# Performance work log

Hardware: AMD Instinct MI355X
Metric: run time of the kernel (lower is better)

Reference implementation:

```python
import jax, jax.numpy as jnp
from jax import lax
import numpy as np

B, T, D_IN, H, OUT = 64, 512, 512, 1024, 128


def setup_inputs() -> dict:
    key = jax.random.key(0)
    ks = jax.random.split(key, 12)
    s = 0.02
    return {
        "x": jax.random.normal(ks[0], (B, T, D_IN), dtype=jnp.float32),
        "W_ih0": jax.random.normal(ks[1], (H, D_IN), dtype=jnp.float32) * s,
        "W_hh0": jax.random.normal(ks[2], (H, H), dtype=jnp.float32) * s,
        "b_ih0": jax.random.normal(ks[3], (H,), dtype=jnp.float32) * s,
        "b_hh0": jax.random.normal(ks[4], (H,), dtype=jnp.float32) * s,
        "W_ih1": jax.random.normal(ks[5], (H, H), dtype=jnp.float32) * s,
        "W_hh1": jax.random.normal(ks[6], (H, H), dtype=jnp.float32) * s,
        "b_ih1": jax.random.normal(ks[7], (H,), dtype=jnp.float32) * s,
        "b_hh1": jax.random.normal(ks[8], (H,), dtype=jnp.float32) * s,
        "W_fc": jax.random.normal(ks[9], (OUT, H), dtype=jnp.float32) * s,
        "b_fc": jax.random.normal(ks[10], (OUT,), dtype=jnp.float32) * s,
    }


def _rnn_layer(seq, W_ih, W_hh, b_ih, b_hh):
    # seq: [B, T, D] -> outputs [B, T, H]; h_t = tanh(x_t W_ih^T + b_ih + h_{t-1} W_hh^T + b_hh)
    pre = jnp.einsum("btd,hd->bth", seq, W_ih) + b_ih + b_hh  # one big input GEMM
    h0 = jnp.zeros((seq.shape[0], W_hh.shape[0]), dtype=seq.dtype)

    def step(h, p_t):
        h_new = jnp.tanh(p_t + h @ W_hh.T)
        return h_new, h_new

    _, hs = lax.scan(step, h0, jnp.swapaxes(pre, 0, 1))  # [T, B, H]
    return jnp.swapaxes(hs, 0, 1)  # [B, T, H]


def reference(x, W_ih0, W_hh0, b_ih0, b_hh0, W_ih1, W_hh1, b_ih1, b_hh1, W_fc, b_fc):
    h1 = _rnn_layer(x, W_ih0, W_hh0, b_ih0, b_hh0)
    h2 = _rnn_layer(h1, W_ih1, W_hh1, b_ih1, b_hh1)
    last = h2[:, -1, :]  # [B, H]
    return last @ W_fc.T + b_fc  # [B, OUT]
```

## Files before the change

### kernel.cpp

```cpp
#include <hip/hip_runtime.h>
#include <stdint.h>
#include <stddef.h>

#define Bn   64
#define Tn   512
#define DINn 512
#define Hn   1024
#define OUTn 128

typedef __attribute__((ext_vector_type(4))) float f32x4;
typedef __attribute__((ext_vector_type(8))) short short8;
typedef __attribute__((ext_vector_type(4))) unsigned int u32x4;

__device__ __forceinline__ unsigned short f2bf(float f){
  unsigned int x = __builtin_bit_cast(unsigned int, f);
  x += 0x7fffu + ((x >> 16) & 1u);
  return (unsigned short)(x >> 16);
}
__device__ __forceinline__ float bf2f(unsigned short u){
  return __builtin_bit_cast(float, (unsigned int)u << 16);
}
__device__ __forceinline__ float tanh_fast(float v){
  float e = __expf(2.0f * v);
  return 1.0f - 2.0f / (e + 1.0f);
}

#define LGKM_BAR() asm volatile("s_waitcnt lgkmcnt(0)\ns_barrier" ::: "memory")

template<bool FAST>
__device__ __forceinline__ void st16(unsigned short* p, u32x4 v){
  if constexpr (FAST)
    asm volatile("global_store_dwordx4 %0, %1, off sc0" :: "v"(p), "v"(v) : "memory");
  else
    asm volatile("global_store_dwordx4 %0, %1, off sc0 sc1" :: "v"(p), "v"(v) : "memory");
}
__device__ __forceinline__ unsigned atom_poll(unsigned int* p){
  unsigned old, zero = 0;
  asm volatile("global_atomic_add %0, %1, %2, off sc0\n\t"
               "s_waitcnt vmcnt(0)"
               : "=&v"(old) : "v"(p), "v"(zero) : "memory");
  return old;
}
__device__ __forceinline__ void atom_poll2(unsigned int* p1, unsigned int* p2,
                                           unsigned &v1, unsigned &v2){
  unsigned zero = 0;
  asm volatile("global_atomic_add %0, %2, %4, off sc0\n\t"
               "global_atomic_add %1, %3, %4, off sc0\n\t"
               "s_waitcnt vmcnt(0)"
               : "=&v"(v1), "=&v"(v2)
               : "v"(p1), "v"(p2), "v"(zero) : "memory");
}
__device__ __forceinline__ void atom_inc(unsigned int* p){
  unsigned one = 1;
  asm volatile("global_atomic_add %0, %1, off" :: "v"(p), "v"(one) : "memory");
}
__device__ __forceinline__ unsigned ld1_sc0(const unsigned int* p){
  unsigned v;
  asm volatile("global_load_dword %0, %1, off sc0\n\t"
               "s_waitcnt vmcnt(0)" : "=&v"(v) : "v"(p) : "memory");
  return v;
}
__device__ __forceinline__ unsigned ld1_nt(const unsigned int* p){
  unsigned v;
  asm volatile("global_load_dword %0, %1, off nt\n\t"
               "s_waitcnt vmcnt(0)" : "=&v"(v) : "v"(p) : "memory");
  return v;
}
__device__ __forceinline__ void ld2_nt(const unsigned int* p1, const unsigned int* p2,
                                       unsigned &v1, unsigned &v2){
  asm volatile("global_load_dword %0, %2, off nt\n\t"
               "global_load_dword %1, %3, off nt\n\t"
               "s_waitcnt vmcnt(0)"
               : "=&v"(v1), "=&v"(v2) : "v"(p1), "v"(p2) : "memory");
}
__device__ __forceinline__ unsigned umin4(u32x4 a){
  unsigned m0 = a[0] < a[1] ? a[0] : a[1];
  unsigned m1 = a[2] < a[3] ? a[2] : a[3];
  return m0 < m1 ? m0 : m1;
}
__device__ __forceinline__ unsigned ld_line8_slow(const unsigned int* p){
  u32x4 a, b;
  asm volatile("global_load_dwordx4 %0, %2, off sc0 sc1\n\t"
               "global_load_dwordx4 %1, %3, off sc0 sc1\n\t"
               "s_waitcnt vmcnt(0)"
               : "=&v"(a), "=&v"(b) : "v"(p), "v"(p + 4) : "memory");
  unsigned ma = umin4(a), mb = umin4(b);
  return ma < mb ? ma : mb;
}
__device__ __forceinline__ void waitw_nt(const unsigned int* p, unsigned want){
  if (!want) return;
  for (int i = 0; i < (1 << 16); ++i){
    if (ld1_nt(p) >= want) return;
    if (i > 16) __builtin_amdgcn_s_sleep(1);
  }
}
__device__ __forceinline__ void waitw_nt2(const unsigned int* p1, unsigned w1,
                                          const unsigned int* p2, unsigned w2){
  if (!w1){ waitw_nt(p2, w2); return; }
  for (int i = 0; i < (1 << 16); ++i){
    unsigned v1, v2;
    ld2_nt(p1, p2, v1, v2);
    if (v1 >= w1 && v2 >= w2) return;
    if (i > 16) __builtin_amdgcn_s_sleep(1);
  }
}
template<bool FAST>
__device__ __forceinline__ void wait_one(unsigned int* fc, unsigned int* fl, unsigned wfast, unsigned wslow){
  if constexpr (FAST){
    if (!wfast) return;
    for (int i = 0; i < (1 << 16); ++i){
      if (atom_poll(fc) >= wfast) return;
      if (i > 8) __builtin_amdgcn_s_sleep(1);
    }
  } else {
    if (!wslow) return;
    for (int i = 0; i < (1 << 16); ++i){
      if (ld_line8_slow(fl) >= wslow) return;
      if (i > 16) __builtin_amdgcn_s_sleep(1);
    }
  }
}
template<bool FAST>
__device__ __forceinline__ void wait_dual(unsigned int* fc1, unsigned int* fl1, unsigned wf1, unsigned ws1,
                                          unsigned int* fc2, unsigned int* fl2, unsigned wf2, unsigned ws2){
  if constexpr (FAST){
    if (!wf2){ wait_one<true>(fc1, fl1, wf1, ws1); return; }
    for (int i = 0; i < (1 << 16); ++i){
      unsigned v1, v2;
      atom_poll2(fc1, fc2, v1, v2);
      if (v1 >= wf1 && v2 >= wf2) return;
      if (i > 8) __builtin_amdgcn_s_sleep(1);
    }
  } else {
    if (!ws2){ wait_one<false>(fc1, fl1, wf1, ws1); return; }
    for (int i = 0; i < (1 << 16); ++i){
      if (ld_line8_slow(fl1) >= ws1 && ld_line8_slow(fl2) >= ws2) return;
      if (i > 16) __builtin_amdgcn_s_sleep(1);
    }
  }
}

__device__ __forceinline__ bool chk8(u32x4 v){
  bool ok = true;
#pragma unroll
  for (int d = 0; d < 4; ++d){
    ok = ok && ((v[d] & 0xFFFFu) != 0xFFFFu) && ((v[d] >> 16) != 0xFFFFu);
  }
  return ok;
}
__device__ __forceinline__ void poison_stage(const unsigned short* src, unsigned short* dst, int lane){
  const unsigned short* p0 = src + lane*8;
  const unsigned short* p1 = p0 + 512;
  u32x4 v0, v1;
  bool ok = false;
  for (int i = 0; i < (1 << 16) && !ok; ++i){
    asm volatile("global_load_dwordx4 %0, %2, off nt\n\t"
                 "global_load_dwordx4 %1, %3, off nt\n\t"
                 "s_waitcnt vmcnt(0)"
                 : "=&v"(v0), "=&v"(v1) : "v"(p0), "v"(p1) : "memory");
    ok = chk8(v0) && chk8(v1);
    if (!ok && i > 4) __builtin_amdgcn_s_sleep(1);
  }
  *(u32x4*)(dst + lane*8) = v0;
  *(u32x4*)(dst + lane*8 + 512) = v1;
}
__device__ __forceinline__ void poison_pv(const unsigned short* p, float* pv, bool active){
  unsigned u0 = 0, u1 = 0, u2 = 0, u3 = 0;
  bool ok = !active;
  for (int i = 0; i < (1 << 16) && !ok; ++i){
    asm volatile("global_load_ushort %0, %4, off nt\n\t"
                 "global_load_ushort %1, %5, off nt\n\t"
                 "global_load_ushort %2, %6, off nt\n\t"
                 "global_load_ushort %3, %7, off nt\n\t"
                 "s_waitcnt vmcnt(0)"
                 : "=&v"(u0), "=&v"(u1), "=&v"(u2), "=&v"(u3)
                 : "v"(p), "v"(p + 8), "v"(p + 16), "v"(p + 24) : "memory");
    ok = (u0 != 0xFFFFu) && (u1 != 0xFFFFu) && (u2 != 0xFFFFu) && (u3 != 0xFFFFu);
    if (!ok && i > 4) __builtin_amdgcn_s_sleep(1);
  }
  pv[0] = bf2f((unsigned short)u0); pv[1] = bf2f((unsigned short)u1);
  pv[2] = bf2f((unsigned short)u2); pv[3] = bf2f((unsigned short)u3);
}

__device__ __forceinline__ void stage_pw(const unsigned short* src, unsigned short* dst, int lane){
  const unsigned short* p0 = src + lane*8;
  const unsigned short* p1 = p0 + 512;
  u32x4 v0, v1;
  asm volatile("global_load_dwordx4 %0, %2, off sc0\n\t"
               "global_load_dwordx4 %1, %3, off sc0\n\t"
               "s_waitcnt vmcnt(0)"
               : "=&v"(v0), "=&v"(v1) : "v"(p0), "v"(p1) : "memory");
  *(u32x4*)(dst + lane*8) = v0;
  *(u32x4*)(dst + lane*8 + 512) = v1;
}
__device__ __forceinline__ void stage_pw_pv(const unsigned short* src, unsigned short* dst, int lane,
                                            const unsigned short* p4, float* pv){
  const unsigned short* p0 = src + lane*8;
  const unsigned short* p1 = p0 + 512;
  u32x4 v0, v1; unsigned u0,u1,u2,u3;
  asm volatile(
    "global_load_dwordx4 %0, %6, off sc0\n\t"
    "global_load_dwordx4 %1, %7, off sc0\n\t"
    "global_load_ushort %2, %8, off sc0\n\t"
    "global_load_ushort %3, %9, off sc0\n\t"
    "global_load_ushort %4, %10, off sc0\n\t"
    "global_load_ushort %5, %11, off sc0\n\t"
    "s_waitcnt vmcnt(0)"
    : "=&v"(v0),"=&v"(v1),"=&v"(u0),"=&v"(u1),"=&v"(u2),"=&v"(u3)
    : "v"(p0),"v"(p1),"v"(p4),"v"(p4+8),"v"(p4+16),"v"(p4+24) : "memory");
  *(u32x4*)(dst + lane*8) = v0;
  *(u32x4*)(dst + lane*8 + 512) = v1;
  pv[0]=bf2f((unsigned short)u0); pv[1]=bf2f((unsigned short)u1);
  pv[2]=bf2f((unsigned short)u2); pv[3]=bf2f((unsigned short)u3);
}

template<bool FAST>
__device__ __forceinline__ void stage_lin(const unsigned short* base, unsigned short* hl, int tid){
  const unsigned short* p0 = base + (size_t)tid * 8;
  const unsigned short* p1 = p0 + 4096;
  u32x4 v0, v1;
  if constexpr (FAST)
    asm volatile("global_load_dwordx4 %0, %2, off sc0\n\t"
                 "global_load_dwordx4 %1, %3, off sc0\n\t"
                 "s_waitcnt vmcnt(0)"
                 : "=&v"(v0), "=&v"(v1) : "v"(p0), "v"(p1) : "memory");
  else
    asm volatile("global_load_dwordx4 %0, %2, off sc0 sc1\n\t"
                 "global_load_dwordx4 %1, %3, off sc0 sc1\n\t"
                 "s_waitcnt vmcnt(0)"
                 : "=&v"(v0), "=&v"(v1) : "v"(p0), "v"(p1) : "memory");
  *(u32x4*)((char*)hl + tid * 16) = v0;
  *(u32x4*)((char*)hl + tid * 16 + 8192) = v1;
}
template<bool FAST>
__device__ __forceinline__ void ld4_chunk(const unsigned short* p, float* pv){
  unsigned u0,u1,u2,u3;
  if constexpr (FAST)
    asm volatile("global_load_ushort %0, %4, off sc0\n\t"
                 "global_load_ushort %1, %5, off sc0\n\t"
                 "global_load_ushort %2, %6, off sc0\n\t"
                 "global_load_ushort %3, %7, off sc0\n\t"
                 "s_waitcnt vmcnt(0)"
                 : "=&v"(u0), "=&v"(u1), "=&v"(u2), "=&v"(u3)
                 : "v"(p), "v"(p + 8), "v"(p + 16), "v"(p + 24) : "memory");
  else
    asm volatile("global_load_ushort %0, %4, off sc0 sc1\n\t"
                 "global_load_ushort %1, %5, off sc0 sc1\n\t"
                 "global_load_ushort %2, %6, off sc0 sc1\n\t"
                 "global_load_ushort %3, %7, off sc0 sc1\n\t"
                 "s_waitcnt vmcnt(0)"
                 : "=&v"(u0), "=&v"(u1), "=&v"(u2), "=&v"(u3)
                 : "v"(p), "v"(p + 8), "v"(p + 16), "v"(p + 24) : "memory");
  pv[0] = bf2f((unsigned short)u0); pv[1] = bf2f((unsigned short)u1);
  pv[2] = bf2f((unsigned short)u2); pv[3] = bf2f((unsigned short)u3);
}

__device__ __forceinline__ f32x4 mfma_tile(const char* lbase, const short8* wf, int lrow, int kh){
  f32x4 a0 = {0.f,0.f,0.f,0.f}, a1 = a0, a2 = a0, a3 = a0;
  int rb = kh * 128 + lrow * 16;
#pragma unroll
  for (int kk = 0; kk < 8; ++kk)
    a0 = __builtin_amdgcn_mfma_f32_16x16x32_bf16(*(const short8*)(lbase + kk*512 + rb), wf[kk], a0, 0,0,0);
#pragma unroll
  for (int kk = 8; kk < 16; ++kk)
    a1 = __builtin_amdgcn_mfma_f32_16x16x32_bf16(*(const short8*)(lbase + kk*512 + rb), wf[kk], a1, 0,0,0);
#pragma unroll
  for (int kk = 16; kk < 24; ++kk)
    a2 = __builtin_amdgcn_mfma_f32_16x16x32_bf16(*(const short8*)(lbase + kk*512 + rb), wf[kk], a2, 0,0,0);
#pragma unroll
  for (int kk = 24; kk < 32; ++kk)
    a3 = __builtin_amdgcn_mfma_f32_16x16x32_bf16(*(const short8*)(lbase + kk*512 + rb), wf[kk], a3, 0,0,0);
  return (a0 + a1) + (a2 + a3);
}

__global__ void cvt_bf16x8(const float* __restrict__ in, unsigned short* __restrict__ out,
                           long long n8){
  long long i = (long long)blockIdx.x * blockDim.x + threadIdx.x;
  long long stride = (long long)gridDim.x * blockDim.x;
  for (; i < n8; i += stride){
    const float* p = in + i*8;
    float4 a = *(const float4*)p;
    float4 b = *(const float4*)(p+4);
    short8 v;
    v[0]=(short)f2bf(a.x); v[1]=(short)f2bf(a.y); v[2]=(short)f2bf(a.z); v[3]=(short)f2bf(a.w);
    v[4]=(short)f2bf(b.x); v[5]=(short)f2bf(b.y); v[6]=(short)f2bf(b.z); v[7]=(short)f2bf(b.w);
    *(short8*)(out + i*8) = v;
  }
}

__global__ void bias_combine(const float* __restrict__ a, const float* __restrict__ b, float* __restrict__ o,
                             const float* __restrict__ c, const float* __restrict__ d, float* __restrict__ p){
  int i = blockIdx.x * blockDim.x + threadIdx.x;
  if (i < Hn){ o[i] = a[i] + b[i]; p[i] = c[i] + d[i]; }
}

__launch_bounds__(256, 2)
__global__ void gemm_pre0(const float* __restrict__ Av, const unsigned short* __restrict__ Bm,
                          const float* __restrict__ bias, unsigned short* __restrict__ C,
                          int N, int K)
{
  __shared__ unsigned short lA[128*64];
  __shared__ unsigned short lB[128*64];
  int bn = blockIdx.x, bm = blockIdx.y;
  int m0 = bm*128, n0 = bn*128;
  int tid = threadIdx.x, lane = tid & 63, w = tid >> 6;
  int wm = (w >> 1)*64, wn = (w & 1)*64;
  int cl = lane & 15, kh = lane >> 4;

  f32x4 acc[4][4];
  f32x4 z = {0.f,0.f,0.f,0.f};
#pragma unroll
  for (int i=0;i<4;i++)
#pragma unroll
    for (int j=0;j<4;j++) acc[i][j]=z;

  for (int k0 = 0; k0 < K; k0 += 64){
    __syncthreads();
#pragma unroll
    for (int r = 0; r < 4; ++r){
      int c = r*256 + tid;
      int row = c >> 3, cof = (c & 7)*8;
      const float* ap = Av + (size_t)(m0+row)*K + k0 + cof;
      float4 a = *(const float4*)ap;
      float4 b = *(const float4*)(ap+4);
      short8 v;
      v[0]=(short)f2bf(a.x); v[1]=(short)f2bf(a.y); v[2]=(short)f2bf(a.z); v[3]=(short)f2bf(a.w);
      v[4]=(short)f2bf(b.x); v[5]=(short)f2bf(b.y); v[6]=(short)f2bf(b.z); v[7]=(short)f2bf(b.w);
      *(short8*)&lA[row*64 + cof] = v;
      const unsigned short* bp = Bm + (size_t)(n0+row)*K + k0 + cof;
      *(short8*)&lB[row*64 + cof] = *(const short8*)bp;
    }
    __syncthreads();
#pragma unroll
    for (int kk = 0; kk < 2; ++kk){
      int kb = kk*32 + kh*8;
      short8 af[4], bfr[4];
#pragma unroll
      for (int i=0;i<4;i++) af[i]  = *(const short8*)&lA[(wm + i*16 + cl)*64 + kb];
#pragma unroll
      for (int j=0;j<4;j++) bfr[j] = *(const short8*)&lB[(wn + j*16 + cl)*64 + kb];
#pragma unroll
      for (int i=0;i<4;i++)
#pragma unroll
        for (int j=0;j<4;j++)
          acc[i][j] = __builtin_amdgcn_mfma_f32_16x16x32_bf16(af[i], bfr[j], acc[i][j], 0,0,0);
    }
  }
#pragma unroll
  for (int j=0;j<4;j++){
    int n = n0 + wn + j*16 + cl;
    float bs = bias[n];
#pragma unroll
    for (int i=0;i<4;i++){
      int mr = m0 + wm + i*16 + kh*4;
#pragma unroll
      for (int e=0;e<4;e++){
        int m = mr + e;
        int b = m >> 9, t = m & (Tn-1);
        C[((size_t)t*Bn + b)*N + n] = f2bf(acc[i][j][e] + bs);
      }
    }
  }
}

template<int MODE, bool POISON>
__device__ __forceinline__ void rnn_body(
    int role, int g, int slot, int tid, int w, int lane, int cl, int kh, int lrow,
    const unsigned short* pre0, unsigned short* h1base, unsigned short* pre1base,
    unsigned short* h2base, const float* bias1,
    unsigned int* FCA0, unsigned int* FCA1, unsigned int* FCB, unsigned int* FCC,
    unsigned int* FLA, unsigned int* FLB, unsigned int* FLC,
    unsigned int* FNA, unsigned int* FNB, unsigned int* FNC,
    const short8* wf, unsigned short* hl, unsigned short* outl)
{
  constexpr bool FAST = (MODE < 2);
  const char* lbase = (const char*)hl;
  int n0 = slot*128 + w*16;
  int olocal = w*128 + ((cl>>3)*8 + kh*4)*8 + (cl&7);
  int khc = kh & 1;
  unsigned int* myFL = ((role == 0) ? FLA : (role == 1) ? FLB : FLC) + slot;
  unsigned int* myFN = ((role == 0) ? FNA : (role == 1) ? FNB : FNC) + slot;

  for (int t = 0; t < Tn; ++t){
    float pv[4] = {0.f,0.f,0.f,0.f};
    if (role == 0 && kh < 2){
      const unsigned short* pp = pre0 + ((size_t)t*Bn + g*8 + kh*4)*Hn + n0 + cl;
#pragma unroll
      for (int j=0;j<4;j++) pv[j] = bf2f(pp[(size_t)j*Hn]);
    }
    bool staged = true;
    if constexpr (MODE == 0 && POISON){
      if (role == 0){
        if (t > 0) poison_stage(h1base + ((size_t)(t+1)*8 + g)*8192 + w*1024, hl + w*1024, lane);
        else staged = false;
      } else if (role == 1){
        poison_stage(h1base + ((size_t)(t+2)*8 + g)*8192 + w*1024, hl + w*1024, lane);
      } else {
        const unsigned short* pA = pre1base + ((size_t)t*8 + g)*8192 + slot*1024
                                   + ((w*16+cl)>>3)*64 + khc*32 + (cl&7);
        if (t > 0) poison_stage(h2base + ((size_t)(t-1)*8 + g)*8192 + w*1024, hl + w*1024, lane);
        else staged = false;
        poison_pv(pA, pv, kh < 2);
      }
    } else if constexpr (MODE == 0){
      if (role == 0){
        if (t > 0){
          waitw_nt(FNA + w, (unsigned)t);
          stage_pw(h1base + ((size_t)(t+1)*8 + g)*8192 + w*1024, hl + w*1024, lane);
        } else staged = false;
      } else if (role == 1){
        waitw_nt(FNA + w, (unsigned)(t+1));
        stage_pw(h1base + ((size_t)(t+2)*8 + g)*8192 + w*1024, hl + w*1024, lane);
      } else {
        const unsigned short* pA = pre1base + ((size_t)t*8 + g)*8192 + slot*1024
                                   + ((w*16+cl)>>3)*64 + khc*32 + (cl&7);
        if (t > 0){
          waitw_nt2(FNC + w, (unsigned)t, FNB + slot, (unsigned)(t+1));
          stage_pw_pv(h2base + ((size_t)(t-1)*8 + g)*8192 + w*1024, hl + w*1024, lane, pA, pv);
        } else {
          staged = false;
          waitw_nt(FNB + slot, 1u);
          ld4_chunk<true>(pA, pv);
        }
      }
    } else {
      if (tid == 0){
        if (role == 0)      wait_one <FAST>(FCA0, FLA, 8u*(unsigned)t, (unsigned)t);
        else if (role == 1) wait_one <FAST>(FCA1, FLA, 8u*(unsigned)(t+1), (unsigned)(t+1));
        else                wait_dual<FAST>(FCB, FLB, 8u*(unsigned)(t+1), (unsigned)(t+1),
                                            FCC, FLC, 8u*(unsigned)t, (unsigned)t);
      }
      __syncthreads();
      if (role == 0){
        if (t > 0) stage_lin<FAST>(h1base + ((size_t)(t+1)*8 + g)*8192, hl, tid);
        else staged = false;
      } else if (role == 1){
        stage_lin<FAST>(h1base + ((size_t)(t+2)*8 + g)*8192, hl, tid);
      } else {
        if (kh < 2)
          ld4_chunk<FAST>(pre1base + ((size_t)t*8 + g)*8192 + slot*1024 + ((w*16+cl)>>3)*64 + kh*32 + (cl&7), pv);
        if (t > 0) stage_lin<FAST>(h2base + ((size_t)(t-1)*8 + g)*8192, hl, tid);
        else staged = false;
      }
    }
    if constexpr (MODE == 0 && POISON) LGKM_BAR();
    else __syncthreads();
    f32x4 acc = {0.f,0.f,0.f,0.f};
    if (staged) acc = mfma_tile(lbase, wf, lrow, kh);
    if (kh < 2){
      float bs = (role == 1) ? bias1[n0 + cl] : 0.f;
#pragma unroll
      for (int j=0;j<4;j++){
        float v = acc[j] + pv[j] + bs;
        if (role != 1) v = tanh_fast(v);
        outl[olocal + j*8] = f2bf(v);
      }
    }
    unsigned short* tile;
    if (role == 0)      tile = h1base + ((size_t)(t+2)*8 + g)*8192;
    else if (role == 1) tile = pre1base + ((size_t)t*8 + g)*8192;
    else                tile = h2base + ((size_t)t*8 + g)*8192;
    if (lane < 16){
      u32x4 v = *(const u32x4*)(outl + w*128 + lane*8);
      st16<FAST>(tile + slot*1024 + (w*16 + lane)*8, v);
    }
    if constexpr (MODE == 0 && POISON){
      LGKM_BAR();
    } else {
      asm volatile("s_waitcnt vmcnt(0)" ::: "memory");
      __syncthreads();
      if constexpr (MODE == 0){
        if (lane == 0 && w == 0)
          asm volatile("global_store_dword %0, %1, off sc0" :: "v"(myFN), "v"((unsigned)(t+1)) : "memory");
      } else if constexpr (MODE == 1){
        if (tid == 0){
          if (role == 0){ atom_inc(FCA0); atom_inc(FCA1); }
          else if (role == 1) atom_inc(FCB);
          else atom_inc(FCC);
        }
      } else {
        if (tid == 0)
          asm volatile("global_store_dword %0, %1, off sc0 sc1" :: "v"(myFL), "v"((unsigned)(t+1)) : "memory");
      }
    }
  }
}

__launch_bounds__(512, 2)
__global__ void rnn_fused(const unsigned short* __restrict__ pre0_ro,
                          unsigned short* __restrict__ h1base,
                          unsigned short* __restrict__ pre1base,
                          unsigned short* __restrict__ h2base,
                          const float* __restrict__ Whh0,
                          const float* __restrict__ Wih1,
                          const float* __restrict__ Whh1,
                          const float* __restrict__ bias1,
                          unsigned int* ctrs, int allowPoison)
{
  __shared__ __align__(16) unsigned short hl[8192];
  __shared__ __align__(16) unsigned short outl[1024];
  __shared__ int s_mode;
  int bx = blockIdx.x;
  int g = bx & 7;
  int sub = bx >> 3;
  int role = sub >> 3, slot = sub & 7;
  int tid = threadIdx.x, lane = tid & 63, w = tid >> 6;
  int n0 = slot*128 + w*16;
  int cl = lane & 15, kh = lane >> 4, lrow = cl & 7;
  unsigned int* FLA = ctrs + (0*8 + g)*32;
  unsigned int* FLB = ctrs + (1*8 + g)*32;
  unsigned int* FLC = ctrs + (2*8 + g)*32;
  unsigned int* arrive1 = ctrs + 768;
  unsigned int* badAT   = ctrs + 772;
  unsigned int* arrive2 = ctrs + 776;
  unsigned int* badNT   = ctrs + 780;
  unsigned int* arrive3 = ctrs + 784;
  unsigned int* FCA0 = ctrs + 1536 + (0*8 + g)*32;
  unsigned int* FCB  = ctrs + 1536 + (1*8 + g)*32;
  unsigned int* FCC  = ctrs + 1536 + (2*8 + g)*32;
  unsigned int* FCA1 = ctrs + 1536 + (3*8 + g)*32;
  unsigned int* FNA = ctrs + 2560 + (0*8 + g)*32;
  unsigned int* FNB = ctrs + 2560 + (1*8 + g)*32;
  unsigned int* FNC = ctrs + 2560 + (2*8 + g)*32;

  if (tid == 0){
    int xcc;
    asm volatile("s_getreg_b32 %0, hwreg(HW_REG_XCC_ID)" : "=s"(xcc));
    unsigned int* atw = ctrs + 1024 + g*32;  unsigned int* atarmed = atw + 16;
    unsigned int* ntw = ctrs + 3328 + g*32;  unsigned int* ntarmed = ntw + 16;
    if (xcc != g){
      __hip_atomic_fetch_or(badNT, 1u, __ATOMIC_RELAXED, __HIP_MEMORY_SCOPE_AGENT);
      __hip_atomic_fetch_or(badAT, 1u, __ATOMIC_RELAXED, __HIP_MEMORY_SCOPE_AGENT);
    }
    unsigned pr = ld1_nt(ntw) + ld1_nt(ntarmed);
    asm volatile("" :: "v"(pr));
    __hip_atomic_fetch_add(arrive1, 1u, __ATOMIC_ACQ_REL, __HIP_MEMORY_SCOPE_AGENT);
    int t1 = 0;
    for (int i = 0; i < (1 << 20); ++i){
      if (__hip_atomic_load(arrive1, __ATOMIC_ACQUIRE, __HIP_MEMORY_SCOPE_AGENT) >= 192u){ t1 = 1; break; }
      __builtin_amdgcn_s_sleep(2);
    }
    if (!t1){
      __hip_atomic_fetch_or(badNT, 1u, __ATOMIC_RELAXED, __HIP_MEMORY_SCOPE_AGENT);
      __hip_atomic_fetch_or(badAT, 1u, __ATOMIC_RELAXED, __HIP_MEMORY_SCOPE_AGENT);
    }
    unsigned magicN = 0xBEEF0000u | (unsigned)g;
    if (sub == 0){
      asm volatile("global_store_dword %0, %1, off sc0\n\t"
                   "s_waitcnt vmcnt(0)\n\t"
                   "global_store_dword %2, %3, off sc0"
                   :: "v"(ntw), "v"(magicN), "v"(ntarmed), "v"(1u) : "memory");
    }
    int okN = 0;
    for (int i = 0; i < (1 << 14); ++i){
      if (ld1_nt(ntarmed) == 1u){ okN = (ld1_nt(ntw) == magicN); break; }
      if (i > 8) __builtin_amdgcn_s_sleep(1);
    }
    if (!okN) __hip_atomic_fetch_or(badNT, 1u, __ATOMIC_RELAXED, __HIP_MEMORY_SCOPE_AGENT);
    __hip_atomic_fetch_add(arrive2, 1u, __ATOMIC_ACQ_REL, __HIP_MEMORY_SCOPE_AGENT);
    int t2 = 0;
    for (int i = 0; i < (1 << 20); ++i){
      if (__hip_atomic_load(arrive2, __ATOMIC_ACQUIRE, __HIP_MEMORY_SCOPE_AGENT) >= 192u){ t2 = 1; break; }
      __builtin_amdgcn_s_sleep(2);
    }
    if (!t2){
      __hip_atomic_fetch_or(badNT, 1u, __ATOMIC_RELAXED, __HIP_MEMORY_SCOPE_AGENT);
      __hip_atomic_fetch_or(badAT, 1u, __ATOMIC_RELAXED, __HIP_MEMORY_SCOPE_AGENT);
    }
    unsigned magicA = 0xCAFE0000u | (unsigned)g;
    if (sub == 0){
      asm volatile("global_store_dword %0, %1, off sc0\n\t"
                   "s_waitcnt vmcnt(0)" :: "v"(atw), "v"(magicA) : "memory");
      atom_inc(atarmed);
    }
    int okA = 0;
    for (int i = 0; i < (1 << 15); ++i){
      if (atom_poll(atarmed) >= 1u){ okA = (ld1_sc0(atw) == magicA); break; }
      if (i > 16) __builtin_amdgcn_s_sleep(1);
    }
    if (!okA) __hip_atomic_fetch_or(badAT, 1u, __ATOMIC_RELAXED, __HIP_MEMORY_SCOPE_AGENT);
    __hip_atomic_fetch_add(arrive3, 1u, __ATOMIC_ACQ_REL, __HIP_MEMORY_SCOPE_AGENT);
    int t3 = 0;
    for (int i = 0; i < (1 << 20); ++i){
      if (__hip_atomic_load(arrive3, __ATOMIC_ACQUIRE, __HIP_MEMORY_SCOPE_AGENT) >= 192u){ t3 = 1; break; }
      __builtin_amdgcn_s_sleep(2);
    }
    unsigned bN = __hip_atomic_load(badNT, __ATOMIC_ACQUIRE, __HIP_MEMORY_SCOPE_AGENT);
    unsigned bA = __hip_atomic_load(badAT, __ATOMIC_ACQUIRE, __HIP_MEMORY_SCOPE_AGENT);
    s_mode = (!t3) ? 2 : (bN == 0u ? 0 : (bA == 0u ? 1 : 2));
  }
  __syncthreads();
  const int mode = s_mode;

  const float* Wmat = (role == 0) ? Whh0 : (role == 1) ? Wih1 : Whh1;
  short8 wf[32];
  {
    const float* wr = Wmat + (size_t)(n0 + cl)*Hn + kh*8;
#pragma unroll
    for (int kk = 0; kk < 32; ++kk){
      float4 a = *(const float4*)(wr + kk*32);
      float4 b = *(const float4*)(wr + kk*32 + 4);
      short8 v;
      v[0]=(short)f2bf(a.x); v[1]=(short)f2bf(a.y); v[2]=(short)f2bf(a.z); v[3]=(short)f2bf(a.w);
      v[4]=(short)f2bf(b.x); v[5]=(short)f2bf(b.y); v[6]=(short)f2bf(b.z); v[7]=(short)f2bf(b.w);
      wf[kk] = v;
    }
  }

  if (mode == 0 && allowPoison)
    rnn_body<0,true >(role, g, slot, tid, w, lane, cl, kh, lrow, pre0_ro, h1base, pre1base, h2base,
                      bias1, FCA0, FCA1, FCB, FCC, FLA, FLB, FLC, FNA, FNB, FNC, wf, hl, outl);
  else if (mode == 0)
    rnn_body<0,false>(role, g, slot, tid, w, lane, cl, kh, lrow, pre0_ro, h1base, pre1base, h2base,
                      bias1, FCA0, FCA1, FCB, FCC, FLA, FLB, FLC, FNA, FNB, FNC, wf, hl, outl);
  else if (mode == 1)
    rnn_body<1,false>(role, g, slot, tid, w, lane, cl, kh, lrow, pre0_ro, h1base, pre1base, h2base,
                      bias1, FCA0, FCA1, FCB, FCC, FLA, FLB, FLC, FNA, FNB, FNC, wf, hl, outl);
  else
    rnn_body<2,false>(role, g, slot, tid, w, lane, cl, kh, lrow, pre0_ro, h1base, pre1base, h2base,
                      bias1, FCA0, FCA1, FCB, FCC, FLA, FLB, FLC, FNA, FNB, FNC, wf, hl, outl);
}

__global__ void fc_k(const unsigned short* __restrict__ h2base,
                     const float* __restrict__ Wfc, const float* __restrict__ bfc,
                     float* __restrict__ out)
{
  int gw = (blockIdx.x * blockDim.x + threadIdx.x) >> 6;
  int lane = threadIdx.x & 63;
  int b = gw >> 7, o = gw & 127;
  const unsigned short* tile = h2base + ((size_t)(Tn-1)*8 + (b>>3))*8192;
  int r = b & 7;
  const float* wr = Wfc + (size_t)o*Hn;
  float s = 0.f;
  for (int k = lane; k < Hn; k += 64)
    s += bf2f(tile[((k>>3)*8 + r)*8 + (k&7)]) * wr[k];
#pragma unroll
  for (int off = 32; off > 0; off >>= 1) s += __shfl_down(s, off, 64);
  if (lane == 0) out[b*OUTn + o] = s + bfc[o];
}

extern "C" void kernel_launch(void* const* d_in, const int* in_sizes, int n_in,
                              void* d_out, int out_size, void* d_ws, size_t ws_size,
                              hipStream_t stream)
{
  const float* x    = (const float*)d_in[0];
  const float* Wih0 = (const float*)d_in[1];
  const float* Whh0 = (const float*)d_in[2];
  const float* bih0 = (const float*)d_in[3];
  const float* bhh0 = (const float*)d_in[4];
  const float* Wih1 = (const float*)d_in[5];
  const float* Whh1 = (const float*)d_in[6];
  const float* bih1 = (const float*)d_in[7];
  const float* bhh1 = (const float*)d_in[8];
  const float* Wfc  = (const float*)d_in[9];
  const float* bfc  = (const float*)d_in[10];
  float* out = (float*)d_out;

  const size_t nP  = (size_t)Bn*Tn*Hn;
  const size_t nH1 = (size_t)(Tn+2)*8*8192;
  const size_t nT  = (size_t)Tn*8*8192;
  const size_t nW  = (size_t)Hn*DINn;

  size_t needP = (nP + nH1 + 2*nT + nW)*2 + 2*Hn*sizeof(float) + 8192*sizeof(unsigned);
  int poison = (ws_size >= needP + 4096) ? 1 : 0;

  unsigned short* bufP  = (unsigned short*)d_ws;
  unsigned short* h1buf = bufP  + nP;
  unsigned short* pre1b;
  unsigned short* h2b;
  unsigned short* wih0b;
  if (poison){
    pre1b = h1buf + nH1;
    h2b   = pre1b + nT;
    wih0b = h2b + nT;
  } else {
    pre1b = h1buf;
    h2b   = bufP;
    wih0b = h1buf + nH1;
  }
  float* bias0 = (float*)(wih0b + nW);
  float* bias1 = bias0 + Hn;
  unsigned int* ctrs = (unsigned int*)(bias1 + Hn);

  hipMemsetAsync(ctrs, 0, 4096*sizeof(unsigned int), stream);
  if (poison){
    hipMemsetAsync(h1buf, 0xFF, nH1*2, stream);
    hipMemsetAsync(pre1b, 0xFF, nT*2, stream);
    hipMemsetAsync(h2b,   0xFF, nT*2, stream);
  }

  cvt_bf16x8<<<256, 256, 0, stream>>>(Wih0, wih0b, (long long)(nW/8));
  bias_combine<<<4, 256, 0, stream>>>(bih0, bhh0, bias0, bih1, bhh1, bias1);

  dim3 g1(Hn/128, (Bn*Tn)/128);
  gemm_pre0<<<g1, 256, 0, stream>>>(x, wih0b, bias0, bufP, Hn, DINn);

  rnn_fused<<<192, 512, 0, stream>>>(bufP, h1buf, pre1b, h2b,
                                     Whh0, Wih1, Whh1, bias1, ctrs, poison);

  fc_k<<<2048, 256, 0, stream>>>(h2b, Wfc, bfc, out);
}
```

Baseline: 1.148 ms.

## Reuse pre0 buffer for h2 with in-kernel poisoning, double-buffer LDS

In the poison-based sync mode, layer-0 blocks now overwrite the consumed pre0 entries with the 0xFFFF poison value after reading them. This lets the h2 buffer alias the pre0 buffer and drops one large hipMemsetAsync plus a workspace region. LDS staging and output buffers are double-buffered by timestep parity, so the trailing LDS barrier at the end of each step can be removed. The cost is extra global stores and vmcnt waits in role-0 blocks, doubled shared memory (which may limit occupancy), and correctness that depends on the ordering between the poison stores and later h2 writes.

```diff
diff --git a/kernel.cpp b/kernel.cpp
--- a/kernel.cpp
+++ b/kernel.cpp
@@ -374,7 +374,6 @@
     const short8* wf, unsigned short* hl, unsigned short* outl)
 {
   constexpr bool FAST = (MODE < 2);
-  const char* lbase = (const char*)hl;
   int n0 = slot*128 + w*16;
   int olocal = w*128 + ((cl>>3)*8 + kh*4)*8 + (cl&7);
   int khc = kh & 1;
@@ -382,23 +381,41 @@
   unsigned int* myFN = ((role == 0) ? FNA : (role == 1) ? FNB : FNC) + slot;
 
   for (int t = 0; t < Tn; ++t){
+    int obuf = (MODE == 0 && POISON) ? (t & 1) : 0;
+    unsigned short* hlb = hl + obuf*8192;
+    unsigned short* olb = outl + obuf*1024;
+    const char* lbase = (const char*)hlb;
+
     float pv[4] = {0.f,0.f,0.f,0.f};
+    const unsigned short* pp = nullptr;
     if (role == 0 && kh < 2){
-      const unsigned short* pp = pre0 + ((size_t)t*Bn + g*8 + kh*4)*Hn + n0 + cl;
+      pp = pre0 + ((size_t)t*Bn + g*8 + kh*4)*Hn + n0 + cl;
 #pragma unroll
       for (int j=0;j<4;j++) pv[j] = bf2f(pp[(size_t)j*Hn]);
     }
     bool staged = true;
     if constexpr (MODE == 0 && POISON){
       if (role == 0){
-        if (t > 0) poison_stage(h1base + ((size_t)(t+1)*8 + g)*8192 + w*1024, hl + w*1024, lane);
-        else staged = false;
+        asm volatile("s_waitcnt vmcnt(0)" ::: "memory");
+        if (kh < 2){
+          unsigned short* pz = (unsigned short*)pp;
+          unsigned pzv = 0xFFFFu;
+#pragma unroll
+          for (int j=0;j<4;j++)
+            asm volatile("global_store_short %0, %1, off sc0" :: "v"(pz + (size_t)j*Hn), "v"(pzv) : "memory");
+        }
+        if (t > 0){
+          poison_stage(h1base + ((size_t)(t+1)*8 + g)*8192 + w*1024, hlb + w*1024, lane);
+        } else {
+          staged = false;
+          asm volatile("s_waitcnt vmcnt(0)" ::: "memory");
+        }
       } else if (role == 1){
-        poison_stage(h1base + ((size_t)(t+2)*8 + g)*8192 + w*1024, hl + w*1024, lane);
+        poison_stage(h1base + ((size_t)(t+2)*8 + g)*8192 + w*1024, hlb + w*1024, lane);
       } else {
         const unsigned short* pA = pre1base + ((size_t)t*8 + g)*8192 + slot*1024
                                    + ((w*16+cl)>>3)*64 + khc*32 + (cl&7);
-        if (t > 0) poison_stage(h2base + ((size_t)(t-1)*8 + g)*8192 + w*1024, hl + w*1024, lane);
+        if (t > 0) poison_stage(h2base + ((size_t)(t-1)*8 + g)*8192 + w*1024, hlb + w*1024, lane);
         else staged = false;
         poison_pv(pA, pv, kh < 2);
       }
@@ -406,17 +423,17 @@
       if (role == 0){
         if (t > 0){
           waitw_nt(FNA + w, (unsigned)t);
-          stage_pw(h1base + ((size_t)(t+1)*8 + g)*8192 + w*1024, hl + w*1024, lane);
+          stage_pw(h1base + ((size_t)(t+1)*8 + g)*8192 + w*1024, hlb + w*1024, lane);
         } else staged = false;
       } else if (role == 1){
         waitw_nt(FNA + w, (unsigned)(t+1));
-        stage_pw(h1base + ((size_t)(t+2)*8 + g)*8192 + w*1024, hl + w*1024, lane);
+        stage_pw(h1base + ((size_t)(t+2)*8 + g)*8192 + w*1024, hlb + w*1024, lane);
       } else {
         const unsigned short* pA = pre1base + ((size_t)t*8 + g)*8192 + slot*1024
                                    + ((w*16+cl)>>3)*64 + khc*32 + (cl&7);
         if (t > 0){
           waitw_nt2(FNC + w, (unsigned)t, FNB + slot, (unsigned)(t+1));
-          stage_pw_pv(h2base + ((size_t)(t-1)*8 + g)*8192 + w*1024, hl + w*1024, lane, pA, pv);
+          stage_pw_pv(h2base + ((size_t)(t-1)*8 + g)*8192 + w*1024, hlb + w*1024, lane, pA, pv);
         } else {
           staged = false;
           waitw_nt(FNB + slot, 1u);
@@ -432,14 +449,14 @@
       }
       __syncthreads();
       if (role == 0){
-        if (t > 0) stage_lin<FAST>(h1base + ((size_t)(t+1)*8 + g)*8192, hl, tid);
+        if (t > 0) stage_lin<FAST>(h1base + ((size_t)(t+1)*8 + g)*8192, hlb, tid);
         else staged = false;
       } else if (role == 1){
-        stage_lin<FAST>(h1base + ((size_t)(t+2)*8 + g)*8192, hl, tid);
+        stage_lin<FAST>(h1base + ((size_t)(t+2)*8 + g)*8192, hlb, tid);
       } else {
         if (kh < 2)
           ld4_chunk<FAST>(pre1base + ((size_t)t*8 + g)*8192 + slot*1024 + ((w*16+cl)>>3)*64 + kh*32 + (cl&7), pv);
-        if (t > 0) stage_lin<FAST>(h2base + ((size_t)(t-1)*8 + g)*8192, hl, tid);
+        if (t > 0) stage_lin<FAST>(h2base + ((size_t)(t-1)*8 + g)*8192, hlb, tid);
         else staged = false;
       }
     }
@@ -453,7 +470,7 @@
       for (int j=0;j<4;j++){
         float v = acc[j] + pv[j] + bs;
         if (role != 1) v = tanh_fast(v);
-        outl[olocal + j*8] = f2bf(v);
+        olb[olocal + j*8] = f2bf(v);
       }
     }
     unsigned short* tile;
@@ -461,11 +478,10 @@
     else if (role == 1) tile = pre1base + ((size_t)t*8 + g)*8192;
     else                tile = h2base + ((size_t)t*8 + g)*8192;
     if (lane < 16){
-      u32x4 v = *(const u32x4*)(outl + w*128 + lane*8);
+      u32x4 v = *(const u32x4*)(olb + w*128 + lane*8);
       st16<FAST>(tile + slot*1024 + (w*16 + lane)*8, v);
     }
     if constexpr (MODE == 0 && POISON){
-      LGKM_BAR();
     } else {
       asm volatile("s_waitcnt vmcnt(0)" ::: "memory");
       __syncthreads();
@@ -497,8 +513,8 @@
                           const float* __restrict__ bias1,
                           unsigned int* ctrs, int allowPoison)
 {
-  __shared__ __align__(16) unsigned short hl[8192];
-  __shared__ __align__(16) unsigned short outl[1024];
+  __shared__ __align__(16) unsigned short hl[16384];
+  __shared__ __align__(16) unsigned short outl[2048];
   __shared__ int s_mode;
   int bx = blockIdx.x;
   int g = bx & 7;
@@ -661,21 +677,19 @@
   const size_t nT  = (size_t)Tn*8*8192;
   const size_t nW  = (size_t)Hn*DINn;
 
-  size_t needP = (nP + nH1 + 2*nT + nW)*2 + 2*Hn*sizeof(float) + 8192*sizeof(unsigned);
+  size_t needP = (nP + nH1 + nT + nW)*2 + 2*Hn*sizeof(float) + 8192*sizeof(unsigned);
   int poison = (ws_size >= needP + 4096) ? 1 : 0;
 
   unsigned short* bufP  = (unsigned short*)d_ws;
   unsigned short* h1buf = bufP  + nP;
   unsigned short* pre1b;
-  unsigned short* h2b;
+  unsigned short* h2b = bufP;
   unsigned short* wih0b;
   if (poison){
     pre1b = h1buf + nH1;
-    h2b   = pre1b + nT;
-    wih0b = h2b + nT;
+    wih0b = pre1b + nT;
   } else {
     pre1b = h1buf;
-    h2b   = bufP;
     wih0b = h1buf + nH1;
   }
   float* bias0 = (float*)(wih0b + nW);
@@ -686,7 +700,6 @@
   if (poison){
     hipMemsetAsync(h1buf, 0xFF, nH1*2, stream);
     hipMemsetAsync(pre1b, 0xFF, nT*2, stream);
-    hipMemsetAsync(h2b,   0xFF, nT*2, stream);
   }
 
   cvt_bf16x8<<<256, 256, 0, stream>>>(Wih0, wih0b, (long long)(nW/8));
```

Measured after the change: 1.300 ms. +13.2%, slower.
